# Optimization experiments

Hardware: AMD Instinct MI355X
Metric: run time of the kernel (lower is better)

The kernel has to match this reference:

```python
import jax, jax.numpy as jnp
import numpy as np

WS = 8          # window size
DISP = 4        # ws // 2 cyclic shift displacement
WS2 = WS * WS   # tokens per window
HEADS = 3
HD = 32         # head dim
SCALE = HD ** -0.5


def _mask(upper_lower, left_right):
    m = np.zeros((WS2, WS2), np.float32)
    if upper_lower:
        m[-DISP * WS:, :-DISP * WS] = -np.inf
        m[:-DISP * WS, -DISP * WS:] = -np.inf
    if left_right:
        m = m.reshape(WS, WS, WS, WS)
        m[:, -DISP:, :, :-DISP] = -np.inf
        m[:, :-DISP, :, -DISP:] = -np.inf
        m = m.reshape(WS2, WS2)
    return m

UL = _mask(True, False)
LR = _mask(False, True)
_ix = np.array([(i, j) for i in range(WS) for j in range(WS)])
REL = (_ix[None] - _ix[:, None]) + WS - 1  # [WS2, WS2, 2] relative index table


def _ln(x, g, b):
    m = x.mean(-1, keepdims=True)
    v = ((x - m) ** 2).mean(-1, keepdims=True)
    return (x - m) * jax.lax.rsqrt(v + 1e-5) * g + b


def _wattn(x, Wqkv, pos, Wo, bo, shifted):
    if shifted:
        x = jnp.roll(x, (-DISP, -DISP), axis=(1, 2))
    b, H, W, _ = x.shape
    nh, nw = H // WS, W // WS
    # qkv: last dim laid out as (3, heads, head_dim) matching torch chunk + rearrange
    qkv = (x @ Wqkv).reshape(b, nh, WS, nw, WS, 3, HEADS, HD)
    qkv = qkv.transpose(5, 0, 6, 1, 3, 2, 4, 7).reshape(3, b, HEADS, nh * nw, WS2, HD)
    q, k, v = qkv[0], qkv[1], qkv[2]
    dots = jnp.einsum('bhwid,bhwjd->bhwij', q, k) * SCALE  # [b,h,nwin,ws2,ws2]
    dots = dots + pos[REL[..., 0], REL[..., 1]]            # relative pos bias
    if shifted:
        m = np.zeros((nh * nw, WS2, WS2), np.float32)
        m[-nw:] += UL             # windows in last row
        m[nw - 1::nw] += LR       # windows in last column
        dots = dots + jnp.asarray(m)[None, None]
    a = jax.nn.softmax(dots, axis=-1)
    o = jnp.einsum('bhwij,bhwjd->bhwid', a, v)
    o = o.reshape(b, HEADS, nh, nw, WS, WS, HD).transpose(0, 2, 4, 3, 5, 1, 6).reshape(b, H, W, HEADS * HD)
    o = o @ Wo + bo
    if shifted:
        o = jnp.roll(o, (DISP, DISP), axis=(1, 2))
    return o


def _block(t, g1, b1, Wqkv, pos, Wo, bo, g2, b2, W1, bf1, W2, bf2, shifted):
    t = t + _wattn(_ln(t, g1, b1), Wqkv, pos, Wo, bo, shifted)
    h = _ln(t, g2, b2)
    return t + (jax.nn.gelu(h @ W1 + bf1, approximate=False) @ W2 + bf2)


def _stage(x, Wm, bm, pa, pb):
    b, c, H, W = x.shape
    nh, nw = H // 2, W // 2
    # PatchMerging: Unfold(k=2,s=2) layout is (c, ki, kj) with c outermost
    t = x.reshape(b, c, nh, 2, nw, 2).transpose(0, 2, 4, 1, 3, 5).reshape(b, nh, nw, c * 4)
    t = t @ Wm + bm
    t = _block(t, *pa, False)
    t = _block(t, *pb, True)
    return t.transpose(0, 3, 1, 2)


def setup_inputs() -> dict:
    key = jax.random.key(0)
    ks = jax.random.split(key, 12)
    def w(k, shp):
        return jax.random.normal(k, shp, jnp.float32) * 0.02
    def blk(kw, kp, ko, k1, k2):
        return {'g1': jnp.ones((128,), jnp.float32), 'b1': jnp.zeros((128,), jnp.float32),
                'Wqkv': w(kw, (128, 288)), 'pos': jax.random.normal(kp, (15, 15), jnp.float32),
                'Wo': w(ko, (96, 128)), 'bo': jnp.zeros((128,), jnp.float32),
                'g2': jnp.ones((128,), jnp.float32), 'b2': jnp.zeros((128,), jnp.float32),
                'W1': w(k1, (128, 512)), 'bf1': jnp.zeros((512,), jnp.float32),
                'W2': w(k2, (512, 128)), 'bf2': jnp.zeros((128,), jnp.float32)}
    A = blk(ks[2], ks[3], ks[4], ks[5], ks[6])
    B = blk(ks[7], ks[8], ks[9], ks[10], ks[11])
    inp = {'x': jax.random.normal(ks[0], (8, 64, 256, 256), jnp.float32),
           'Wm': w(ks[1], (256, 128)), 'bm': jnp.zeros((128,), jnp.float32)}
    for n, v in A.items():
        inp[n + 'a'] = v
    for n, v in B.items():
        inp[n + 'b'] = v
    return inp


def reference(x, Wm, bm, g1a, b1a, Wqkva, posa, Woa, boa, g2a, b2a, W1a, bf1a, W2a, bf2a,
              g1b, b1b, Wqkvb, posb, Wob, bob, g2b, b2b, W1b, bf1b, W2b, bf2b):
    pa = (g1a, b1a, Wqkva, posa, Woa, boa, g2a, b2a, W1a, bf1a, W2a, bf2a)
    pb = (g1b, b1b, Wqkvb, posb, Wob, bob, g2b, b2b, W1b, bf1b, W2b, bf2b)
    return _stage(x, Wm, bm, pa, pb)
```

## Files before the change

### kernel.cpp

```cpp
#include <hip/hip_runtime.h>
#include <math.h>

#define Timg 131072
#define SCALE 0.17677669529663689f

typedef __attribute__((ext_vector_type(8))) short frag8;
typedef __attribute__((ext_vector_type(8))) unsigned short us8;
typedef __attribute__((ext_vector_type(4))) float f32x4;

__device__ inline float bf2f(unsigned short u) {
    union { unsigned int i; float f; } v; v.i = ((unsigned int)u) << 16; return v.f;
}
__device__ inline unsigned short f2bf(float f) {
    union { float f; unsigned int i; } v; v.f = f;
    unsigned int r = v.i + 0x7fff + ((v.i >> 16) & 1);
    return (unsigned short)(r >> 16);
}
__device__ inline unsigned int pk2(float lo, float hi) {
    return ((unsigned int)f2bf(hi) << 16) | (unsigned int)f2bf(lo);
}
__device__ inline float gelu_f(float x) {
    float z2 = 1.5957691f * (x + 0.044715f * x * x * x);
    return x * __builtin_amdgcn_rcpf(1.f + __expf(-z2));
}

__global__ __launch_bounds__(256) void k_wcvt(
    const float* __restrict__ src, unsigned short* __restrict__ dst, int R, int C)
{
    int idx = blockIdx.x * 256 + threadIdx.x;
    if (idx >= R * C) return;
    int r = idx / C, c = idx % C;
    dst[(size_t)c * R + r] = f2bf(src[idx]);
}

#define LDA_PM 264
__global__ __launch_bounds__(256) void k_patchmerge(
    const float* __restrict__ x, const unsigned short* __restrict__ Wmt,
    const float* __restrict__ bm, float* __restrict__ t)
{
    __shared__ unsigned short A[64 * LDA_PM];
    int blk = blockIdx.x;
    int b   = blk >> 8;
    int rem = blk & 255;
    int h   = rem >> 1;
    int w0  = (rem & 1) * 64;
    int tid = threadIdx.x;
    {
        int row = tid >> 1, half = tid & 1;
        int c = row >> 1, ki = row & 1;
        const float* src = x + (((size_t)(b*64 + c))*256 + (size_t)(2*h + ki))*256 + 2*w0 + half*64;
        int base = c*4 + ki*2;
        #pragma unroll
        for (int q = 0; q < 16; ++q) {
            float4 v = *reinterpret_cast<const float4*>(src + q*4);
            int tk0 = (half*64 + q*4) >> 1;
            *reinterpret_cast<unsigned int*>(&A[ tk0     * LDA_PM + base]) = pk2(v.x, v.y);
            *reinterpret_cast<unsigned int*>(&A[(tk0 + 1)* LDA_PM + base]) = pk2(v.z, v.w);
        }
    }
    __syncthreads();
    int lane = tid & 63, w = tid >> 6;
    int lr = lane & 15, lg = lane >> 4;
    size_t tok0 = (size_t)blk * 64;
    #pragma unroll
    for (int nt = 0; nt < 2; ++nt) {
        int n0 = (w*2 + nt) * 16;
        f32x4 acc[4] = {};
        #pragma unroll
        for (int ks = 0; ks < 8; ++ks) {
            frag8 bfr = *reinterpret_cast<const frag8*>(Wmt + (size_t)(n0 + lr)*256 + ks*32 + lg*8);
            #pragma unroll
            for (int m = 0; m < 4; ++m) {
                frag8 af = *reinterpret_cast<const frag8*>(&A[(m*16 + lr)*LDA_PM + ks*32 + lg*8]);
                acc[m] = __builtin_amdgcn_mfma_f32_16x16x32_bf16(af, bfr, acc[m], 0, 0, 0);
            }
        }
        #pragma unroll
        for (int m = 0; m < 4; ++m)
            #pragma unroll
            for (int r = 0; r < 4; ++r) {
                int rowl = m*16 + lg*4 + r;
                int col  = n0 + lr;
                t[(tok0 + rowl)*128 + col] = acc[m][r] + bm[col];
            }
    }
}

#define LDQK 200
#define LDVT 72
#define LDP  72
#define LDAO 104
#define LDA  136
#define LDH  136
#define OFF_VT  25600
#define R1SZ    39424
#define OFF_AO  48640
#define SMEMSZ  61952
__global__ __launch_bounds__(256) void k_block(
    const float* __restrict__ pos, float* __restrict__ t,
    const float* __restrict__ g1, const float* __restrict__ b1,
    const unsigned short* __restrict__ Wqt,
    const unsigned short* __restrict__ Wot, const float* __restrict__ bo,
    const float* __restrict__ g2, const float* __restrict__ b2,
    const unsigned short* __restrict__ W1t, const float* __restrict__ bf1,
    const unsigned short* __restrict__ W2t, const float* __restrict__ bf2,
    int shifted)
{
    __shared__ __attribute__((aligned(16))) char smem[SMEMSZ];
    __shared__ float stats[64][4][2];
    __shared__ float ps[225];
    unsigned short* QK   = (unsigned short*)(smem);
    unsigned short* Vt   = (unsigned short*)(smem + OFF_VT);
    unsigned short* Hc   = (unsigned short*)(smem);
    unsigned short* Abuf = (unsigned short*)(smem + R1SZ);
    unsigned short* P    = (unsigned short*)(smem + R1SZ);
    unsigned short* ao   = (unsigned short*)(smem + OFF_AO);

    int blk = blockIdx.x;
    int b   = blk >> 8;
    int win = blk & 255;
    int wy  = win >> 4, wx = win & 15;
    int tid = threadIdx.x, lane = tid & 63, w = tid >> 6;
    int lr  = lane & 15, lg = lane >> 4;
    int sh  = shifted ? 4 : 0;

    for (int idx = tid; idx < 225; idx += 256) ps[idx] = pos[idx];

    #pragma unroll
    for (int it = 0; it < 16; ++it) {
        int m  = w*16 + it;
        int ir = m >> 3, ic = m & 7;
        int hh = (wy*8 + ir + sh) & 127, ww = (wx*8 + ic + sh) & 127;
        const float* p = t + ((size_t)((b*128 + hh)*128 + ww))*128;
        float2 v = *reinterpret_cast<const float2*>(p + lane*2);
        float s = v.x + v.y;
        #pragma unroll
        for (int o = 32; o; o >>= 1) s += __shfl_xor(s, o);
        float mean = s * 0.0078125f;
        float d0 = v.x - mean, d1 = v.y - mean;
        float q = d0*d0 + d1*d1;
        #pragma unroll
        for (int o = 32; o; o >>= 1) q += __shfl_xor(q, o);
        float rs = rsqrtf(q * 0.0078125f + 1e-5f);
        *reinterpret_cast<unsigned int*>(&Abuf[m*LDA + lane*2]) =
            pk2(d0*rs*g1[lane*2] + b1[lane*2], d1*rs*g1[lane*2+1] + b1[lane*2+1]);
    }
    __syncthreads();

    for (int nt = w; nt < 18; nt += 4) {
        f32x4 acc[4] = {};
        #pragma unroll
        for (int ks = 0; ks < 4; ++ks) {
            frag8 bfr = *reinterpret_cast<const frag8*>(Wqt + (size_t)(nt*16 + lr)*128 + ks*32 + lg*8);
            #pragma unroll
            for (int m = 0; m < 4; ++m) {
                frag8 af = *reinterpret_cast<const frag8*>(&Abuf[(m*16 + lr)*LDA + ks*32 + lg*8]);
                acc[m] = __builtin_amdgcn_mfma_f32_16x16x32_bf16(af, bfr, acc[m], 0, 0, 0);
            }
        }
        if (nt < 6) {
            #pragma unroll
            for (int m = 0; m < 4; ++m)
                #pragma unroll
                for (int r = 0; r < 4; ++r)
                    QK[(m*16 + lg*4 + r)*LDQK + nt*16 + lr] = f2bf(acc[m][r] * SCALE);
        } else if (nt < 12) {
            #pragma unroll
            for (int m = 0; m < 4; ++m)
                #pragma unroll
                for (int r = 0; r < 4; ++r)
                    QK[(m*16 + lg*4 + r)*LDQK + nt*16 + lr] = f2bf(acc[m][r]);
        } else {
            #pragma unroll
            for (int m = 0; m < 4; ++m)
                #pragma unroll
                for (int r = 0; r < 4; ++r)
                    Vt[((nt - 12)*16 + lr)*LDVT + (m*16 + lg*4 + r)] = f2bf(acc[m][r]);
        }
    }
    __syncthreads();

    bool mUL = (shifted != 0) && (wy == 15);
    bool mLR = (shifted != 0) && (wx == 15);
    for (int h = 0; h < 3; ++h) {
        frag8 qf = *reinterpret_cast<const frag8*>(&QK[(w*16 + lr)*LDQK + h*32 + lg*8]);
        f32x4 s[4];
        #pragma unroll
        for (int jt = 0; jt < 4; ++jt) {
            frag8 kf = *reinterpret_cast<const frag8*>(&QK[(jt*16 + lr)*LDQK + 96 + h*32 + lg*8]);
            f32x4 z = {0.f, 0.f, 0.f, 0.f};
            s[jt] = __builtin_amdgcn_mfma_f32_16x16x32_bf16(qf, kf, z, 0, 0, 0);
        }
        #pragma unroll
        for (int r = 0; r < 4; ++r) {
            int i  = w*16 + lg*4 + r;
            int ir = i >> 3, ic = i & 7;
            int ro = (7 - ir)*15 + (7 - ic);
            float vals[4]; float mx = -1e30f;
            #pragma unroll
            for (int jt = 0; jt < 4; ++jt) {
                int j = jt*16 + lr, jr = j >> 3, jc = j & 7;
                float val = s[jt][r] + ps[ro + jr*15 + jc];
                if ((mUL && ((jr >= 4) != (ir >= 4))) || (mLR && ((jc >= 4) != (ic >= 4)))) val = -1e30f;
                vals[jt] = val; mx = fmaxf(mx, val);
            }
            #pragma unroll
            for (int o = 8; o; o >>= 1) mx = fmaxf(mx, __shfl_xor(mx, o));
            float sum = 0.f;
            #pragma unroll
            for (int jt = 0; jt < 4; ++jt) { vals[jt] = __expf(vals[jt] - mx); sum += vals[jt]; }
            #pragma unroll
            for (int o = 8; o; o >>= 1) sum += __shfl_xor(sum, o);
            float inv = __builtin_amdgcn_rcpf(sum);
            #pragma unroll
            for (int jt = 0; jt < 4; ++jt)
                P[i*LDP + jt*16 + lr] = f2bf(vals[jt] * inv);
        }
        __syncthreads();
        #pragma unroll
        for (int nd = 0; nd < 2; ++nd) {
            f32x4 o4 = {0.f, 0.f, 0.f, 0.f};
            #pragma unroll
            for (int kt = 0; kt < 2; ++kt) {
                frag8 pf = *reinterpret_cast<const frag8*>(&P[(w*16 + lr)*LDP + kt*32 + lg*8]);
                frag8 vf = *reinterpret_cast<const frag8*>(&Vt[(h*32 + nd*16 + lr)*LDVT + kt*32 + lg*8]);
                o4 = __builtin_amdgcn_mfma_f32_16x16x32_bf16(pf, vf, o4, 0, 0, 0);
            }
            #pragma unroll
            for (int r = 0; r < 4; ++r)
                ao[(w*16 + lg*4 + r)*LDAO + h*32 + nd*16 + lr] = f2bf(o4[r]);
        }
        __syncthreads();
    }
    __syncthreads();

    f32x4 pacc[2][4] = {};
    #pragma unroll
    for (int ks = 0; ks < 3; ++ks) {
        frag8 bw0 = *reinterpret_cast<const frag8*>(Wot + (size_t)(w*32      + lr)*96 + ks*32 + lg*8);
        frag8 bw1 = *reinterpret_cast<const frag8*>(Wot + (size_t)(w*32 + 16 + lr)*96 + ks*32 + lg*8);
        #pragma unroll
        for (int m = 0; m < 4; ++m) {
            frag8 af = *reinterpret_cast<const frag8*>(&ao[(m*16 + lr)*LDAO + ks*32 + lg*8]);
            pacc[0][m] = __builtin_amdgcn_mfma_f32_16x16x32_bf16(af, bw0, pacc[0][m], 0, 0, 0);
            pacc[1][m] = __builtin_amdgcn_mfma_f32_16x16x32_bf16(af, bw1, pacc[1][m], 0, 0, 0);
        }
    }
    float t1[2][4][4];
    int   toks[4][4];
    #pragma unroll
    for (int m = 0; m < 4; ++m)
        #pragma unroll
        for (int r = 0; r < 4; ++r) {
            int rowl = m*16 + lg*4 + r;
            int ir = rowl >> 3, ic = rowl & 7;
            int hh = (wy*8 + ir + sh) & 127, ww = (wx*8 + ic + sh) & 127;
            toks[m][r] = (b*128 + hh)*128 + ww;
            #pragma unroll
            for (int nt = 0; nt < 2; ++nt) {
                int col = w*32 + nt*16 + lr;
                t1[nt][m][r] = t[(size_t)toks[m][r]*128 + col] + pacc[nt][m][r] + bo[col];
            }
        }
    #pragma unroll
    for (int m = 0; m < 4; ++m)
        #pragma unroll
        for (int r = 0; r < 4; ++r) {
            float v0 = t1[0][m][r], v1 = t1[1][m][r];
            float s = v0 + v1, q = v0*v0 + v1*v1;
            #pragma unroll
            for (int o = 8; o; o >>= 1) { s += __shfl_xor(s, o); q += __shfl_xor(q, o); }
            if (lr == 0) {
                int rowl = m*16 + lg*4 + r;
                stats[rowl][w][0] = s;
                stats[rowl][w][1] = q;
            }
        }
    __syncthreads();
    #pragma unroll
    for (int m = 0; m < 4; ++m)
        #pragma unroll
        for (int r = 0; r < 4; ++r) {
            int rowl = m*16 + lg*4 + r;
            float s = 0.f, q = 0.f;
            #pragma unroll
            for (int ww2 = 0; ww2 < 4; ++ww2) { s += stats[rowl][ww2][0]; q += stats[rowl][ww2][1]; }
            float mean = s * 0.0078125f;
            float var  = fmaxf(q * 0.0078125f - mean*mean, 0.f);
            float rs   = rsqrtf(var + 1e-5f);
            #pragma unroll
            for (int nt = 0; nt < 2; ++nt) {
                int col = w*32 + nt*16 + lr;
                Abuf[rowl*LDA + col] = f2bf((t1[nt][m][r] - mean)*rs*g2[col] + b2[col]);
            }
        }
    f32x4 acc2[2][4] = {};
    for (int kc = 0; kc < 4; ++kc) {
        __syncthreads();
        #pragma unroll
        for (int nt = 0; nt < 2; ++nt) {
            int n0 = kc*128 + w*32 + nt*16;
            f32x4 a1[4] = {};
            #pragma unroll
            for (int ks = 0; ks < 4; ++ks) {
                frag8 bfr = *reinterpret_cast<const frag8*>(W1t + (size_t)(n0 + lr)*128 + ks*32 + lg*8);
                #pragma unroll
                for (int m = 0; m < 4; ++m) {
                    frag8 af = *reinterpret_cast<const frag8*>(&Abuf[(m*16 + lr)*LDA + ks*32 + lg*8]);
                    a1[m] = __builtin_amdgcn_mfma_f32_16x16x32_bf16(af, bfr, a1[m], 0, 0, 0);
                }
            }
            #pragma unroll
            for (int m = 0; m < 4; ++m)
                #pragma unroll
                for (int r = 0; r < 4; ++r) {
                    int rowl = m*16 + lg*4 + r;
                    int col  = w*32 + nt*16 + lr;
                    float xv = a1[m][r] + bf1[kc*128 + col];
                    Hc[rowl*LDH + col] = f2bf(gelu_f(xv));
                }
        }
        __syncthreads();
        #pragma unroll
        for (int nt = 0; nt < 2; ++nt) {
            int n0 = w*32 + nt*16;
            #pragma unroll
            for (int ks = 0; ks < 4; ++ks) {
                frag8 bfr = *reinterpret_cast<const frag8*>(W2t + (size_t)(n0 + lr)*512 + kc*128 + ks*32 + lg*8);
                #pragma unroll
                for (int m = 0; m < 4; ++m) {
                    frag8 hf = *reinterpret_cast<const frag8*>(&Hc[(m*16 + lr)*LDH + ks*32 + lg*8]);
                    acc2[nt][m] = __builtin_amdgcn_mfma_f32_16x16x32_bf16(hf, bfr, acc2[nt][m], 0, 0, 0);
                }
            }
        }
    }
    #pragma unroll
    for (int nt = 0; nt < 2; ++nt)
        #pragma unroll
        for (int m = 0; m < 4; ++m)
            #pragma unroll
            for (int r = 0; r < 4; ++r) {
                int col = w*32 + nt*16 + lr;
                t[(size_t)toks[m][r]*128 + col] = t1[nt][m][r] + acc2[nt][m][r] + bf2[col];
            }
}

__global__ __launch_bounds__(256) void k_transpose(
    const float* __restrict__ t, float* __restrict__ out)
{
    __shared__ float tile[128][33];
    int blk = blockIdx.x;
    int ct = blk & 3;
    int h  = (blk >> 2) & 127;
    int b  = blk >> 9;
    const float* src = t + ((size_t)b*16384 + (size_t)h*128)*128 + ct*32;
    #pragma unroll
    for (int q = 0; q < 16; ++q) {
        int idx = threadIdx.x + q*256;
        int w = idx >> 5, c = idx & 31;
        tile[w][c] = src[(size_t)w*128 + c];
    }
    __syncthreads();
    float* dst = out + ((size_t)(b*128 + ct*32))*16384 + (size_t)h*128;
    #pragma unroll
    for (int q = 0; q < 16; ++q) {
        int idx = threadIdx.x + q*256;
        int c = idx >> 7, w = idx & 127;
        dst[(size_t)c*16384 + w] = tile[w][c];
    }
}

extern "C" void kernel_launch(void* const* d_in, const int* in_sizes, int n_in,
                              void* d_out, int out_size, void* d_ws, size_t ws_size,
                              hipStream_t stream)
{
    const float* x  = (const float*)d_in[0];
    const float* Wm = (const float*)d_in[1];
    const float* bm = (const float*)d_in[2];

    float* t           = (float*)d_ws;
    unsigned short* wb = (unsigned short*)(t + (size_t)Timg*128);

    unsigned short* Wmt = wb;
    unsigned short* Wqt[2], *Wot[2], *W1t[2], *W2t[2];
    unsigned short* p = wb + 32768;
    for (int i = 0; i < 2; ++i) {
        Wqt[i] = p; p += 36864;
        Wot[i] = p; p += 12288;
        W1t[i] = p; p += 65536;
        W2t[i] = p; p += 65536;
    }

    k_wcvt<<<(256*128 + 255)/256, 256, 0, stream>>>(Wm, Wmt, 256, 128);
    for (int i = 0; i < 2; ++i) {
        k_wcvt<<<(128*288 + 255)/256, 256, 0, stream>>>((const float*)d_in[ 5 + i*12], Wqt[i], 128, 288);
        k_wcvt<<<( 96*128 + 255)/256, 256, 0, stream>>>((const float*)d_in[ 7 + i*12], Wot[i],  96, 128);
        k_wcvt<<<(128*512 + 255)/256, 256, 0, stream>>>((const float*)d_in[11 + i*12], W1t[i], 128, 512);
        k_wcvt<<<(512*128 + 255)/256, 256, 0, stream>>>((const float*)d_in[13 + i*12], W2t[i], 512, 128);
    }

    k_patchmerge<<<Timg/64, 256, 0, stream>>>(x, Wmt, bm, t);

    for (int blk = 0; blk < 2; ++blk) {
        const float* g1  = (const float*)d_in[ 3 + blk*12];
        const float* b1  = (const float*)d_in[ 4 + blk*12];
        const float* pos = (const float*)d_in[ 6 + blk*12];
        const float* bo  = (const float*)d_in[ 8 + blk*12];
        const float* g2  = (const float*)d_in[ 9 + blk*12];
        const float* b2  = (const float*)d_in[10 + blk*12];
        const float* bf1 = (const float*)d_in[12 + blk*12];
        const float* bf2 = (const float*)d_in[14 + blk*12];

        k_block<<<2048, 256, 0, stream>>>(pos, t, g1, b1, Wqt[blk],
                                          Wot[blk], bo, g2, b2,
                                          W1t[blk], bf1, W2t[blk], bf2, blk);
    }

    k_transpose<<<8*128*4, 256, 0, stream>>>(t, (float*)d_out);
}
```

Measured before the change: 421.7 us.

## Use hardware bf16 pack, fold q-scale into weights, double-buffer MLP hidden, drop barriers

Replaces the software round-to-nearest bf16 conversion with the v_cvt_pk_bf16_f32 instruction. Folds the attention scale into the Q columns of the converted QKV weights and rewrites GELU with exp2. Double-buffers the MLP hidden chunk so each iteration needs one barrier instead of two. Removes the per-head barriers in the attention loop on the assumption that each wave only touches its own P and ao rows. The cost is reliance on the wave-private access pattern and a small rounding difference from scaling Q before the bf16 cast.

```diff
diff --git a/kernel.cpp b/kernel.cpp
--- a/kernel.cpp
+++ b/kernel.cpp
@@ -16,21 +16,31 @@
     unsigned int r = v.i + 0x7fff + ((v.i >> 16) & 1);
     return (unsigned short)(r >> 16);
 }
-__device__ inline unsigned int pk2(float lo, float hi) {
-    return ((unsigned int)f2bf(hi) << 16) | (unsigned int)f2bf(lo);
+__device__ inline unsigned int cvtpk(float lo, float hi) {
+    unsigned int r;
+    asm("v_cvt_pk_bf16_f32 %0, %1, %2" : "=v"(r) : "v"(lo), "v"(hi));
+    return r;
+}
+__device__ inline unsigned short cvt1(float x) {
+    return (unsigned short)cvtpk(x, x);
 }
 __device__ inline float gelu_f(float x) {
-    float z2 = 1.5957691f * (x + 0.044715f * x * x * x);
-    return x * __builtin_amdgcn_rcpf(1.f + __expf(-z2));
+    float u = x * x;
+    float z = x * fmaf(u, 0.044715f, 1.0f);
+    float e = __builtin_amdgcn_exp2f(-2.3025851f * z);
+    return x * __builtin_amdgcn_rcpf(1.f + e);
 }
 
 __global__ __launch_bounds__(256) void k_wcvt(
-    const float* __restrict__ src, unsigned short* __restrict__ dst, int R, int C)
+    const float* __restrict__ src, unsigned short* __restrict__ dst, int R, int C,
+    int qrows, float s)
 {
     int idx = blockIdx.x * 256 + threadIdx.x;
     if (idx >= R * C) return;
     int r = idx / C, c = idx % C;
-    dst[(size_t)c * R + r] = f2bf(src[idx]);
+    float v = src[idx];
+    if (c < qrows) v *= s;
+    dst[(size_t)c * R + r] = cvt1(v);
 }
 
 #define LDA_PM 264
@@ -54,8 +64,8 @@
         for (int q = 0; q < 16; ++q) {
             float4 v = *reinterpret_cast<const float4*>(src + q*4);
             int tk0 = (half*64 + q*4) >> 1;
-            *reinterpret_cast<unsigned int*>(&A[ tk0     * LDA_PM + base]) = pk2(v.x, v.y);
-            *reinterpret_cast<unsigned int*>(&A[(tk0 + 1)* LDA_PM + base]) = pk2(v.z, v.w);
+            *reinterpret_cast<unsigned int*>(&A[ tk0     * LDA_PM + base]) = cvtpk(v.x, v.y);
+            *reinterpret_cast<unsigned int*>(&A[(tk0 + 1)* LDA_PM + base]) = cvtpk(v.z, v.w);
         }
     }
     __syncthreads();
@@ -93,6 +103,7 @@
 #define LDA  136
 #define LDH  136
 #define OFF_VT  25600
+#define OFF_HC1 17408
 #define R1SZ    39424
 #define OFF_AO  48640
 #define SMEMSZ  61952
@@ -111,7 +122,8 @@
     __shared__ float ps[225];
     unsigned short* QK   = (unsigned short*)(smem);
     unsigned short* Vt   = (unsigned short*)(smem + OFF_VT);
-    unsigned short* Hc   = (unsigned short*)(smem);
+    unsigned short* Hc0  = (unsigned short*)(smem);
+    unsigned short* Hc1  = (unsigned short*)(smem + OFF_HC1);
     unsigned short* Abuf = (unsigned short*)(smem + R1SZ);
     unsigned short* P    = (unsigned short*)(smem + R1SZ);
     unsigned short* ao   = (unsigned short*)(smem + OFF_AO);
@@ -143,7 +155,7 @@
         for (int o = 32; o; o >>= 1) q += __shfl_xor(q, o);
         float rs = rsqrtf(q * 0.0078125f + 1e-5f);
         *reinterpret_cast<unsigned int*>(&Abuf[m*LDA + lane*2]) =
-            pk2(d0*rs*g1[lane*2] + b1[lane*2], d1*rs*g1[lane*2+1] + b1[lane*2+1]);
+            cvtpk(d0*rs*g1[lane*2] + b1[lane*2], d1*rs*g1[lane*2+1] + b1[lane*2+1]);
     }
     __syncthreads();
 
@@ -158,30 +170,25 @@
                 acc[m] = __builtin_amdgcn_mfma_f32_16x16x32_bf16(af, bfr, acc[m], 0, 0, 0);
             }
         }
-        if (nt < 6) {
+        if (nt < 12) {
             #pragma unroll
             for (int m = 0; m < 4; ++m)
                 #pragma unroll
                 for (int r = 0; r < 4; ++r)
-                    QK[(m*16 + lg*4 + r)*LDQK + nt*16 + lr] = f2bf(acc[m][r] * SCALE);
-        } else if (nt < 12) {
+                    QK[(m*16 + lg*4 + r)*LDQK + nt*16 + lr] = cvt1(acc[m][r]);
+        } else {
             #pragma unroll
             for (int m = 0; m < 4; ++m)
                 #pragma unroll
                 for (int r = 0; r < 4; ++r)
-                    QK[(m*16 + lg*4 + r)*LDQK + nt*16 + lr] = f2bf(acc[m][r]);
-        } else {
-            #pragma unroll
-            for (int m = 0; m < 4; ++m)
-                #pragma unroll
-                for (int r = 0; r < 4; ++r)
-                    Vt[((nt - 12)*16 + lr)*LDVT + (m*16 + lg*4 + r)] = f2bf(acc[m][r]);
+                    Vt[((nt - 12)*16 + lr)*LDVT + (m*16 + lg*4 + r)] = cvt1(acc[m][r]);
         }
     }
     __syncthreads();
 
     bool mUL = (shifted != 0) && (wy == 15);
     bool mLR = (shifted != 0) && (wx == 15);
+    #pragma unroll 1
     for (int h = 0; h < 3; ++h) {
         frag8 qf = *reinterpret_cast<const frag8*>(&QK[(w*16 + lr)*LDQK + h*32 + lg*8]);
         f32x4 s[4];
@@ -214,9 +221,8 @@
             float inv = __builtin_amdgcn_rcpf(sum);
             #pragma unroll
             for (int jt = 0; jt < 4; ++jt)
-                P[i*LDP + jt*16 + lr] = f2bf(vals[jt] * inv);
-        }
-        __syncthreads();
+                P[i*LDP + jt*16 + lr] = cvt1(vals[jt] * inv);
+        }
         #pragma unroll
         for (int nd = 0; nd < 2; ++nd) {
             f32x4 o4 = {0.f, 0.f, 0.f, 0.f};
@@ -228,9 +234,8 @@
             }
             #pragma unroll
             for (int r = 0; r < 4; ++r)
-                ao[(w*16 + lg*4 + r)*LDAO + h*32 + nd*16 + lr] = f2bf(o4[r]);
-        }
-        __syncthreads();
+                ao[(w*16 + lg*4 + r)*LDAO + h*32 + nd*16 + lr] = cvt1(o4[r]);
+        }
     }
     __syncthreads();
 
@@ -291,12 +296,15 @@
             #pragma unroll
             for (int nt = 0; nt < 2; ++nt) {
                 int col = w*32 + nt*16 + lr;
-                Abuf[rowl*LDA + col] = f2bf((t1[nt][m][r] - mean)*rs*g2[col] + b2[col]);
-            }
-        }
+                Abuf[rowl*LDA + col] = cvt1((t1[nt][m][r] - mean)*rs*g2[col] + b2[col]);
+            }
+        }
+    __syncthreads();
+
     f32x4 acc2[2][4] = {};
+    #pragma unroll 1
     for (int kc = 0; kc < 4; ++kc) {
-        __syncthreads();
+        unsigned short* Hc = (kc & 1) ? Hc1 : Hc0;
         #pragma unroll
         for (int nt = 0; nt < 2; ++nt) {
             int n0 = kc*128 + w*32 + nt*16;
@@ -317,7 +325,7 @@
                     int rowl = m*16 + lg*4 + r;
                     int col  = w*32 + nt*16 + lr;
                     float xv = a1[m][r] + bf1[kc*128 + col];
-                    Hc[rowl*LDH + col] = f2bf(gelu_f(xv));
+                    Hc[rowl*LDH + col] = cvt1(gelu_f(xv));
                 }
         }
         __syncthreads();
@@ -392,12 +400,12 @@
         W2t[i] = p; p += 65536;
     }
 
-    k_wcvt<<<(256*128 + 255)/256, 256, 0, stream>>>(Wm, Wmt, 256, 128);
+    k_wcvt<<<(256*128 + 255)/256, 256, 0, stream>>>(Wm, Wmt, 256, 128, 0, 1.f);
     for (int i = 0; i < 2; ++i) {
-        k_wcvt<<<(128*288 + 255)/256, 256, 0, stream>>>((const float*)d_in[ 5 + i*12], Wqt[i], 128, 288);
-        k_wcvt<<<( 96*128 + 255)/256, 256, 0, stream>>>((const float*)d_in[ 7 + i*12], Wot[i],  96, 128);
-        k_wcvt<<<(128*512 + 255)/256, 256, 0, stream>>>((const float*)d_in[11 + i*12], W1t[i], 128, 512);
-        k_wcvt<<<(512*128 + 255)/256, 256, 0, stream>>>((const float*)d_in[13 + i*12], W2t[i], 512, 128);
+        k_wcvt<<<(128*288 + 255)/256, 256, 0, stream>>>((const float*)d_in[ 5 + i*12], Wqt[i], 128, 288, 96, SCALE);
+        k_wcvt<<<( 96*128 + 255)/256, 256, 0, stream>>>((const float*)d_in[ 7 + i*12], Wot[i],  96, 128, 0, 1.f);
+        k_wcvt<<<(128*512 + 255)/256, 256, 0, stream>>>((const float*)d_in[11 + i*12], W1t[i], 128, 512, 0, 1.f);
+        k_wcvt<<<(512*128 + 255)/256, 256, 0, stream>>>((const float*)d_in[13 + i*12], W2t[i], 512, 128, 0, 1.f);
     }
 
     k_patchmerge<<<Timg/64, 256, 0, stream>>>(x, Wmt, bm, t);
```

Result: slower. 520.7 us (+23.5%).
